# Kernel optimization log

Hardware: AMD Instinct MI355X
Metric: run time of the kernel (lower is better)

Reference implementation:

```python
import jax, jax.numpy as jnp
import numpy as np


def setup_inputs() -> dict:
    key = jax.random.key(0)
    ks = jax.random.split(key, 7)
    B, T, D, H, O = 64, 512, 256, 1024, 256
    s = 0.02  # small init scale for numerical stability of the recurrence
    return {
        "x": jax.random.normal(ks[0], (B, T, D), dtype=jnp.float32),
        "W_ih": jax.random.normal(ks[1], (4 * H, D), dtype=jnp.float32) * s,
        "W_hh": jax.random.normal(ks[2], (4 * H, H), dtype=jnp.float32) * s,
        "b_ih": jax.random.normal(ks[3], (4 * H,), dtype=jnp.float32) * s,
        "b_hh": jax.random.normal(ks[4], (4 * H,), dtype=jnp.float32) * s,
        "W_out": jax.random.normal(ks[5], (O, H), dtype=jnp.float32) * s,
        "b_out": jax.random.normal(ks[6], (O,), dtype=jnp.float32) * s,
    }


def reference(x, W_ih, W_hh, b_ih, b_hh, W_out, b_out):
    # x: [B, T, D]. Faithful to torch nn.LSTMCell gate order (i, f, g, o)
    # followed by a per-step Linear projection, future=0 path.
    B, T, D = x.shape
    H = W_hh.shape[1]

    # Precompute input contributions for all timesteps in one GEMM: [T, B, 4H]
    xg = jnp.einsum('btd,gd->tbg', x, W_ih) + b_ih + b_hh

    def step(carry, xg_t):
        h, c = carry
        gates = xg_t + h @ W_hh.T  # [B, 4H]
        i, f, g, o = jnp.split(gates, 4, axis=-1)
        i = jax.nn.sigmoid(i)
        f = jax.nn.sigmoid(f)
        g = jnp.tanh(g)
        o = jax.nn.sigmoid(o)
        c = f * c + i * g
        h = o * jnp.tanh(c)
        return (h, c), h

    h0 = jnp.zeros((B, H), dtype=x.dtype)
    c0 = jnp.zeros((B, H), dtype=x.dtype)
    _, hs = jax.lax.scan(step, (h0, c0), xg)  # hs: [T, B, H]

    # Per-step Linear, batched over time: [B, T, O]
    outputs = jnp.einsum('tbh,oh->bto', hs, W_out) + b_out
    return outputs
```

## Files before the change

kernel.cpp:

```cpp
#include <hip/hip_runtime.h>

#define B_ 64
#define T_ 512
#define D_ 256
#define H_ 1024
#define O_ 256
#define KTOT 1280
#define NBLK 256
#define NTHR 256

typedef __bf16 bf16x8 __attribute__((ext_vector_type(8)));
typedef float f32x4 __attribute__((ext_vector_type(4)));

__device__ __forceinline__ unsigned short f2bf(float f) {
    unsigned int u = __builtin_bit_cast(unsigned int, f);
    unsigned int r = (u + 0x7fffu + ((u >> 16) & 1u)) >> 16;
    return (unsigned short)r;
}
__device__ __forceinline__ float sigmoid_f(float x) { return 1.f / (1.f + __expf(-x)); }
__device__ __forceinline__ float tanh_f(float x)    { return 1.f - 2.f / (1.f + __expf(2.f * x)); }

#define SYNC_INTS (T_ * 1024 / 4)

__global__ void zero_sync(int* s) { s[blockIdx.x * 256 + threadIdx.x] = 0; }

__global__ __launch_bounds__(256) void pack_weights(
    const float* __restrict__ Wih, const float* __restrict__ Whh,
    const float* __restrict__ bih, const float* __restrict__ bhh,
    const float* __restrict__ Wout,
    unsigned short* __restrict__ Wp, float* __restrict__ bpk,
    unsigned short* __restrict__ Wo)
{
    int bid = blockIdx.x, tid = threadIdx.x;
    if (bid < 4096) {
        int g = bid & 3, hc = bid >> 2;
        int row = g * 1024 + hc;
        for (int e = tid; e < KTOT; e += 256) {
            float v = (e < D_) ? Wih[(size_t)row * D_ + e] : Whh[(size_t)row * H_ + (e - D_)];
            Wp[(size_t)bid * KTOT + e] = f2bf(v);
        }
        if (tid == 0) bpk[bid] = bih[row] + bhh[row];
    } else {
        int r = bid - 4096;
        for (int e = tid; e < H_; e += 256)
            Wo[(size_t)r * H_ + e] = f2bf(Wout[(size_t)r * H_ + e]);
    }
}

__global__ __launch_bounds__(256) void x_pack(const float* __restrict__ x,
                                              unsigned short* __restrict__ xt)
{
    int bid = blockIdx.x;
    int b = bid >> 9, t = bid & 511;
    int d = threadIdx.x;
    xt[((size_t)t * B_ + b) * D_ + d] = f2bf(x[(size_t)bid * D_ + d]);
}

__global__ __launch_bounds__(NTHR, 1) void lstm_scan(
    const unsigned short* __restrict__ Wp, const float* __restrict__ bpk,
    const unsigned short* __restrict__ xt, unsigned short* __restrict__ hs,
    int* __restrict__ sync)
{
    const int tid  = threadIdx.x;
    const int w    = tid >> 6, lane = tid & 63;
    const int blk  = blockIdx.x;
    const int n    = lane & 15, kg = lane >> 4;
    const int gq   = n & 3;
    const int m0   = w * 16;

    unsigned char* arrB = (unsigned char*)sync;

    __shared__ unsigned short st[4][16][4];

    bf16x8 wf[40];
    {
        const bf16x8* wp8 = (const bf16x8*)(Wp + (size_t)(blk * 16 + n) * KTOT + kg * 8);
        #pragma unroll
        for (int kk = 0; kk < 40; ++kk) wf[kk] = wp8[kk * 4];
    }
    #pragma unroll
    for (int kk = 0; kk < 40; ++kk) asm volatile("" : "+v"(wf[kk]));

    const float bias = bpk[blk * 16 + n];

    float cc[4] = {0.f, 0.f, 0.f, 0.f};

    for (int t = 0; t < T_; ++t) {
        f32x4 ac[4];
        f32x4 z = {0.f, 0.f, 0.f, 0.f};
        ac[0] = z; ac[1] = z; ac[2] = z; ac[3] = z;

        {
            const bf16x8* ax = (const bf16x8*)(xt + ((size_t)t * B_ + m0 + n) * D_ + kg * 8);
            #pragma unroll
            for (int kk = 0; kk < 8; ++kk) {
                bf16x8 a = ax[kk * 4];
                ac[kk & 3] = __builtin_amdgcn_mfma_f32_16x16x32_bf16(a, wf[kk], ac[kk & 3], 0, 0, 0);
            }
        }

        if (t > 0) {
            const int* ap = (const int*)(arrB + (size_t)(t - 1) * 1024) + lane * 4;
            for (;;) {
                int v0 = __hip_atomic_load(ap + 0, __ATOMIC_RELAXED, __HIP_MEMORY_SCOPE_AGENT);
                int v1 = __hip_atomic_load(ap + 1, __ATOMIC_RELAXED, __HIP_MEMORY_SCOPE_AGENT);
                int v2 = __hip_atomic_load(ap + 2, __ATOMIC_RELAXED, __HIP_MEMORY_SCOPE_AGENT);
                int v3 = __hip_atomic_load(ap + 3, __ATOMIC_RELAXED, __HIP_MEMORY_SCOPE_AGENT);
                int ok = (v0 == 0x01010101) & (v1 == 0x01010101) &
                         (v2 == 0x01010101) & (v3 == 0x01010101);
                if (__all(ok)) break;
            }

            const bf16x8* ah = (const bf16x8*)(hs + ((size_t)(t - 1) * B_ + m0 + n) * H_ + kg * 8);
            #pragma unroll
            for (int kk = 8; kk < 40; ++kk) {
                bf16x8 a = ah[(kk - 8) * 4];
                ac[kk & 3] = __builtin_amdgcn_mfma_f32_16x16x32_bf16(a, wf[kk], ac[kk & 3], 0, 0, 0);
            }
        }

        f32x4 g4 = (ac[0] + ac[1]) + (ac[2] + ac[3]);

        #pragma unroll
        for (int r = 0; r < 4; ++r) {
            float v   = g4[r] + bias;
            float act = (gq == 2) ? tanh_f(v) : sigmoid_f(v);
            float a1 = __shfl_xor(act, 1);
            float a2 = __shfl_xor(act, 2);
            float a3 = __shfl_xor(act, 3);
            float ia = (gq == 0) ? act : (gq == 1) ? a1 : (gq == 2) ? a2 : a3;
            float fa = (gq == 0) ? a1 : (gq == 1) ? act : (gq == 2) ? a3 : a2;
            float ga = (gq == 0) ? a2 : (gq == 1) ? a3 : (gq == 2) ? act : a1;
            float oa = (gq == 0) ? a3 : (gq == 1) ? a2 : (gq == 2) ? a1 : act;
            float cn = fa * cc[r] + ia * ga;
            cc[r] = cn;
            float hv = oa * tanh_f(cn);
            if (gq == 0) st[w][kg * 4 + r][n >> 2] = f2bf(hv);
        }

        asm volatile("s_waitcnt lgkmcnt(0)" ::: "memory");
        if (lane < 16) {
            unsigned long long pv = *(const unsigned long long*)&st[w][lane][0];
            __hip_atomic_store((unsigned long long*)(hs + ((size_t)t * B_ + m0 + lane) * H_ + blk * 4),
                               pv, __ATOMIC_RELAXED, __HIP_MEMORY_SCOPE_AGENT);
        }
        asm volatile("s_waitcnt vmcnt(0)" ::: "memory");
        if (lane == 0 && t < T_ - 1)
            __hip_atomic_store(arrB + (size_t)t * 1024 + blk * 4 + w, (unsigned char)1,
                               __ATOMIC_RELAXED, __HIP_MEMORY_SCOPE_AGENT);
    }
}

__global__ __launch_bounds__(256) void out_proj(
    const unsigned short* __restrict__ hs, const unsigned short* __restrict__ Wo,
    const float* __restrict__ bout, float* __restrict__ out)
{
    const int tid = threadIdx.x, wid = tid >> 6, lane = tid & 63;
    const int n = lane & 15, kg = lane >> 4;
    const int mb = blockIdx.x >> 2, nb = blockIdx.x & 3;
    const int m0 = mb * 64 + wid * 16;
    const int n0 = nb * 64;
    f32x4 acc[4];
    f32x4 z = {0.f, 0.f, 0.f, 0.f};
    acc[0] = z; acc[1] = z; acc[2] = z; acc[3] = z;
    const bf16x8* ap = (const bf16x8*)(hs + ((size_t)(m0 + n)) * H_ + kg * 8);
    #pragma unroll 2
    for (int kk = 0; kk < 32; ++kk) {
        bf16x8 a = ap[kk * 4];
        #pragma unroll
        for (int nt = 0; nt < 4; ++nt) {
            const bf16x8* bp8 = (const bf16x8*)(Wo + ((size_t)(n0 + nt * 16 + n)) * H_ + kg * 8);
            bf16x8 b = bp8[kk * 4];
            acc[nt] = __builtin_amdgcn_mfma_f32_16x16x32_bf16(a, b, acc[nt], 0, 0, 0);
        }
    }
    #pragma unroll
    for (int nt = 0; nt < 4; ++nt) {
        int col = n0 + nt * 16 + n;
        float bias = bout[col];
        #pragma unroll
        for (int r = 0; r < 4; ++r) {
            int m = m0 + kg * 4 + r;
            int tt = m >> 6, bb = m & 63;
            out[((size_t)bb * T_ + tt) * O_ + col] = acc[nt][r] + bias;
        }
    }
}

extern "C" void kernel_launch(void* const* d_in, const int* in_sizes, int n_in,
                              void* d_out, int out_size, void* d_ws, size_t ws_size,
                              hipStream_t stream)
{
    const float* x    = (const float*)d_in[0];
    const float* Wih  = (const float*)d_in[1];
    const float* Whh  = (const float*)d_in[2];
    const float* bih  = (const float*)d_in[3];
    const float* bhh  = (const float*)d_in[4];
    const float* Wout = (const float*)d_in[5];
    const float* bout = (const float*)d_in[6];
    float* out = (float*)d_out;

    char* ws = (char*)d_ws;
    unsigned short* Wp  = (unsigned short*)ws;  ws += (size_t)4096 * KTOT * 2;
    float*          bpk = (float*)ws;           ws += (size_t)4096 * 4;
    unsigned short* Wo  = (unsigned short*)ws;  ws += (size_t)O_ * H_ * 2;
    unsigned short* xt  = (unsigned short*)ws;  ws += (size_t)T_ * B_ * D_ * 2;
    unsigned short* hs  = (unsigned short*)ws;  ws += (size_t)T_ * B_ * H_ * 2;
    int*            syn = (int*)ws;             ws += (size_t)SYNC_INTS * 4;

    if (ws_size < (size_t)(ws - (char*)d_ws)) return;

    zero_sync<<<SYNC_INTS / 256, 256, 0, stream>>>(syn);
    pack_weights<<<4096 + 256, 256, 0, stream>>>(Wih, Whh, bih, bhh, Wout, Wp, bpk, Wo);
    x_pack<<<B_ * T_, 256, 0, stream>>>(x, xt);

    {
        const unsigned short* Wpc = Wp;
        const float*          bpc = bpk;
        const unsigned short* xtc = xt;
        unsigned short*       hsv = hs;
        int*                  syv = syn;
        void* args[5] = {(void*)&Wpc, (void*)&bpc, (void*)&xtc, (void*)&hsv, (void*)&syv};
        hipLaunchCooperativeKernel((void*)lstm_scan, dim3(NBLK), dim3(NTHR), args, 0, stream);
    }

    out_proj<<<(T_ * B_ / 64) * 4, 256, 0, stream>>>(hs, Wo, bout, out);
}
```

Baseline: 5.147 ms.

## Partition LSTM scan by batch groups so each block waits only on its own group

```diff
diff --git a/kernel.cpp b/kernel.cpp
--- a/kernel.cpp
+++ b/kernel.cpp
@@ -20,7 +20,7 @@
 __device__ __forceinline__ float sigmoid_f(float x) { return 1.f / (1.f + __expf(-x)); }
 __device__ __forceinline__ float tanh_f(float x)    { return 1.f - 2.f / (1.f + __expf(2.f * x)); }
 
-#define SYNC_INTS (T_ * 1024 / 4)
+#define SYNC_INTS (T_ * 4 * 256 / 4)
 
 __global__ void zero_sync(int* s) { s[blockIdx.x * 256 + threadIdx.x] = 0; }
 
@@ -64,24 +64,26 @@
     const int tid  = threadIdx.x;
     const int w    = tid >> 6, lane = tid & 63;
     const int blk  = blockIdx.x;
+    const int g    = blk & 3;
+    const int j    = blk >> 2;
     const int n    = lane & 15, kg = lane >> 4;
     const int gq   = n & 3;
-    const int m0   = w * 16;
+    const int pc   = j * 64 + w * 16 + n;
+    const int hcol = j * 16 + w * 4 + (n >> 2);
+    const int rowb = g * 16;
 
     unsigned char* arrB = (unsigned char*)sync;
-
-    __shared__ unsigned short st[4][16][4];
 
     bf16x8 wf[40];
     {
-        const bf16x8* wp8 = (const bf16x8*)(Wp + (size_t)(blk * 16 + n) * KTOT + kg * 8);
+        const bf16x8* wp8 = (const bf16x8*)(Wp + (size_t)pc * KTOT + kg * 8);
         #pragma unroll
         for (int kk = 0; kk < 40; ++kk) wf[kk] = wp8[kk * 4];
     }
     #pragma unroll
     for (int kk = 0; kk < 40; ++kk) asm volatile("" : "+v"(wf[kk]));
 
-    const float bias = bpk[blk * 16 + n];
+    const float bias = bpk[pc];
 
     float cc[4] = {0.f, 0.f, 0.f, 0.f};
 
@@ -91,7 +93,7 @@
         ac[0] = z; ac[1] = z; ac[2] = z; ac[3] = z;
 
         {
-            const bf16x8* ax = (const bf16x8*)(xt + ((size_t)t * B_ + m0 + n) * D_ + kg * 8);
+            const bf16x8* ax = (const bf16x8*)(xt + ((size_t)t * B_ + rowb + n) * D_ + kg * 8);
             #pragma unroll
             for (int kk = 0; kk < 8; ++kk) {
                 bf16x8 a = ax[kk * 4];
@@ -100,18 +102,16 @@
         }
 
         if (t > 0) {
-            const int* ap = (const int*)(arrB + (size_t)(t - 1) * 1024) + lane * 4;
-            for (;;) {
-                int v0 = __hip_atomic_load(ap + 0, __ATOMIC_RELAXED, __HIP_MEMORY_SCOPE_AGENT);
-                int v1 = __hip_atomic_load(ap + 1, __ATOMIC_RELAXED, __HIP_MEMORY_SCOPE_AGENT);
-                int v2 = __hip_atomic_load(ap + 2, __ATOMIC_RELAXED, __HIP_MEMORY_SCOPE_AGENT);
-                int v3 = __hip_atomic_load(ap + 3, __ATOMIC_RELAXED, __HIP_MEMORY_SCOPE_AGENT);
-                int ok = (v0 == 0x01010101) & (v1 == 0x01010101) &
-                         (v2 == 0x01010101) & (v3 == 0x01010101);
-                if (__all(ok)) break;
+            if (w == 0) {
+                const int* ap = (const int*)(arrB + ((size_t)(t - 1) * 4 + g) * 256) + lane;
+                for (;;) {
+                    int v = __hip_atomic_load(ap, __ATOMIC_RELAXED, __HIP_MEMORY_SCOPE_AGENT);
+                    if (__all(v == 0x01010101)) break;
+                }
             }
-
-            const bf16x8* ah = (const bf16x8*)(hs + ((size_t)(t - 1) * B_ + m0 + n) * H_ + kg * 8);
+            __syncthreads();
+
+            const bf16x8* ah = (const bf16x8*)(hs + ((size_t)(t - 1) * B_ + rowb + n) * H_ + kg * 8);
             #pragma unroll
             for (int kk = 8; kk < 40; ++kk) {
                 bf16x8 a = ah[(kk - 8) * 4];
@@ -121,6 +121,7 @@
 
         f32x4 g4 = (ac[0] + ac[1]) + (ac[2] + ac[3]);
 
+        float hv[4];
         #pragma unroll
         for (int r = 0; r < 4; ++r) {
             float v   = g4[r] + bias;
@@ -134,19 +135,18 @@
             float oa = (gq == 0) ? a3 : (gq == 1) ? a2 : (gq == 2) ? a1 : act;
             float cn = fa * cc[r] + ia * ga;
             cc[r] = cn;
-            float hv = oa * tanh_f(cn);
-            if (gq == 0) st[w][kg * 4 + r][n >> 2] = f2bf(hv);
-        }
-
-        asm volatile("s_waitcnt lgkmcnt(0)" ::: "memory");
-        if (lane < 16) {
-            unsigned long long pv = *(const unsigned long long*)&st[w][lane][0];
-            __hip_atomic_store((unsigned long long*)(hs + ((size_t)t * B_ + m0 + lane) * H_ + blk * 4),
-                               pv, __ATOMIC_RELAXED, __HIP_MEMORY_SCOPE_AGENT);
+            hv[r] = oa * tanh_f(cn);
+        }
+
+        if (gq == 0) {
+            #pragma unroll
+            for (int r = 0; r < 4; ++r)
+                __hip_atomic_store(hs + ((size_t)t * B_ + rowb + kg * 4 + r) * H_ + hcol,
+                                   f2bf(hv[r]), __ATOMIC_RELAXED, __HIP_MEMORY_SCOPE_AGENT);
         }
         asm volatile("s_waitcnt vmcnt(0)" ::: "memory");
         if (lane == 0 && t < T_ - 1)
-            __hip_atomic_store(arrB + (size_t)t * 1024 + blk * 4 + w, (unsigned char)1,
+            __hip_atomic_store(arrB + ((size_t)t * 4 + g) * 256 + j * 4 + w, (unsigned char)1,
                                __ATOMIC_RELAXED, __HIP_MEMORY_SCOPE_AGENT);
     }
 }
```

After: 4.647 ms. 1.11x faster.
